# Kernel tuning notes

Measured on AMD Instinct MI355X. Metric: run time of the kernel, lower is better.

Reference implementation:

```python
import jax, jax.numpy as jnp
import numpy as np

D_STATE = 16


def setup_inputs() -> dict:
    key = jax.random.key(0)
    ks = jax.random.split(key, 7)
    B, S, D = 8, 4096, 64
    ds = D_STATE
    x = jax.random.normal(ks[0], (B, S, D), dtype=jnp.float32)
    # Selection layers modeled as Linear(d_model, out). W_A scaled small so the
    # random transition matrices are contractive over 4096 steps.
    W_A = jax.random.normal(ks[1], (D, ds * ds), dtype=jnp.float32) * 0.01
    b_A = jnp.zeros((ds * ds,), dtype=jnp.float32)
    W_B = jax.random.normal(ks[2], (D, ds * D), dtype=jnp.float32) * 0.05
    b_B = jnp.zeros((ds * D,), dtype=jnp.float32)
    W_C = jax.random.normal(ks[3], (D, ds * D), dtype=jnp.float32) * 0.05
    b_C = jnp.zeros((ds * D,), dtype=jnp.float32)
    return {"x": x, "W_A": W_A, "b_A": b_A, "W_B": W_B, "b_B": b_B,
            "W_C": W_C, "b_C": b_C}


def reference(x, W_A, b_A, W_B, b_B, W_C, b_C):
    B, S, D = x.shape
    ds = D_STATE
    # Input-dependent (selective) parameters per timestep
    A = (x @ W_A + b_A).reshape(B, S, ds, ds)      # [B,S,ds,ds]
    Bm = (x @ W_B + b_B).reshape(B, S, ds, D)      # [B,S,ds,D]
    Cm = (x @ W_C + b_C).reshape(B, S, ds, D)      # [B,S,ds,D]
    # Pre-contract B_t @ x_t once: [B,S,ds]
    Bx = jnp.einsum('bsnd,bsd->bsn', Bm, x)

    def step(h, inputs):
        A_t, Bx_t = inputs                          # [B,ds,ds], [B,ds]
        h = jnp.einsum('bij,bj->bi', A_t, h) + Bx_t
        return h, h

    h0 = jnp.zeros((B, ds), dtype=x.dtype)
    _, hs = jax.lax.scan(step, h0,
                         (jnp.swapaxes(A, 0, 1), jnp.swapaxes(Bx, 0, 1)))
    hs = jnp.swapaxes(hs, 0, 1)                     # [B,S,ds]
    # output_t = C_t^T @ h_t  -> [B,S,D]
    return jnp.einsum('bsnd,bsn->bsd', Cm, hs)
```

## Files before the change

### kernel.cpp

```cpp
#include <hip/hip_runtime.h>

#define BATCH   8
#define SEQ     4096
#define DM      64
#define DS      16
#define BS      (BATCH*SEQ)
#define CHUNK   32
#define NCH     (SEQ/CHUNK)
#define NCH_TOT (BATCH*NCH)
#define SG      16
#define NSG     (NCH_TOT/SG)

typedef __attribute__((ext_vector_type(8))) __bf16 bf16x8;
typedef __attribute__((ext_vector_type(4))) float  f32x4;

__device__ __forceinline__ unsigned short f2bf(float f) {
  unsigned int u = __float_as_uint(f);
  u += 0x7fffu + ((u >> 16) & 1u);
  return (unsigned short)(u >> 16);
}
__device__ __forceinline__ float bflo(unsigned int u) { return __uint_as_float(u << 16); }
__device__ __forceinline__ float bfhi(unsigned int u) { return __uint_as_float(u & 0xffff0000u); }

#define AS_I 20
#define AS_T 324

__global__ __launch_bounds__(256) void k0_cast(
    const float* __restrict__ x, const float* __restrict__ WA,
    const float* __restrict__ WB, const float* __restrict__ WC,
    unsigned short* __restrict__ xb, unsigned short* __restrict__ WAt,
    unsigned short* __restrict__ WBt, unsigned short* __restrict__ WCt)
{
  const int b = blockIdx.x;
  if (b < 1024) {
    const int i = (b * 256 + threadIdx.x) * 8;
    float4 v0 = *(const float4*)(x + i);
    float4 v1 = *(const float4*)(x + i + 4);
    ushort4 o0 = {f2bf(v0.x), f2bf(v0.y), f2bf(v0.z), f2bf(v0.w)};
    ushort4 o1 = {f2bf(v1.x), f2bf(v1.y), f2bf(v1.z), f2bf(v1.w)};
    *(ushort4*)(xb + i)     = o0;
    *(ushort4*)(xb + i + 4) = o1;
  } else {
    const int o = (b - 1024) * 256 + threadIdx.x;
    if (o < 16384) {
      const int c = o >> 6, e = o & 63;
      WAt[o] = f2bf(WA[e * 256 + c]);
    } else if (o < 16384 + 65536) {
      const int p = o - 16384;
      const int c = p >> 6, e = p & 63;
      WBt[p] = f2bf(WB[e * 1024 + c]);
    } else {
      const int p = o - 16384 - 65536;
      const int c = p >> 6, e = p & 63;
      WCt[p] = f2bf(WC[e * 1024 + c]);
    }
  }
}

__global__ __launch_bounds__(256) void g1(
    const unsigned short* __restrict__ xb, const unsigned short* __restrict__ WBt,
    const float* __restrict__ bB, const float* __restrict__ x,
    const unsigned short* __restrict__ WAt, const float* __restrict__ bA,
    unsigned short* __restrict__ Wt_ws, float* __restrict__ u_ws,
    float* __restrict__ P_ws, float* __restrict__ v_ws)
{
  __shared__ __align__(16) unsigned char smem[64 * AS_T * 2];
  float (*xs)[68]     = (float (*)[68])smem;
  float* bBs          = (float*)(smem + 17408);
  unsigned short* As  = (unsigned short*)smem;
  __shared__ __align__(16) float bxs[64][16];
  __shared__ __align__(16) float us[2][16];

  const int tid  = threadIdx.x;
  const int lane = tid & 63;
  const int l15  = lane & 15;
  const int quad = lane >> 4;
  const int w    = tid >> 6;
  const int t0   = blockIdx.x * 64;
  const int twl  = w * 16;

  {
    const float4* xg = (const float4*)(x + (size_t)t0 * DM);
    #pragma unroll
    for (int i = 0; i < 4; ++i) {
      const int f4 = tid + 256 * i;
      ((float4*)&xs[f4 >> 4][0])[f4 & 15] = xg[f4];
    }
    ((float4*)bBs)[tid] = ((const float4*)bB)[tid];
    if (tid < 32) us[tid >> 4][tid & 15] = 0.f;
  }

  const bf16x8* xv = (const bf16x8*)(xb + (size_t)(t0 + twl + l15) * 64);
  bf16x8 a0 = xv[quad];
  bf16x8 a1 = xv[quad + 4];
  __syncthreads();

  #pragma unroll 2
  for (int n = 0; n < 16; ++n) {
    f32x4 ac[4];
    #pragma unroll
    for (int r = 0; r < 4; ++r) {
      const bf16x8* wv = (const bf16x8*)(WBt + (size_t)((n * 4 + r) * 16 + l15) * 64);
      f32x4 t = {0.f, 0.f, 0.f, 0.f};
      t = __builtin_amdgcn_mfma_f32_16x16x32_bf16(a0, wv[quad],     t, 0, 0, 0);
      t = __builtin_amdgcn_mfma_f32_16x16x32_bf16(a1, wv[quad + 4], t, 0, 0, 0);
      ac[r] = t;
    }
    float part[4] = {0.f, 0.f, 0.f, 0.f};
    #pragma unroll
    for (int r = 0; r < 4; ++r) {
      const float bb = bBs[n * 64 + r * 16 + l15];
      #pragma unroll
      for (int reg = 0; reg < 4; ++reg) {
        const int tl = twl + quad * 4 + reg;
        part[reg] = fmaf(ac[r][reg] + bb, xs[tl][r * 16 + l15], part[reg]);
      }
    }
    #pragma unroll
    for (int off = 1; off < 16; off <<= 1) {
      #pragma unroll
      for (int reg = 0; reg < 4; ++reg)
        part[reg] += __shfl_xor(part[reg], off, 64);
    }
    if (l15 == 0) {
      #pragma unroll
      for (int reg = 0; reg < 4; ++reg)
        bxs[twl + quad * 4 + reg][n] = part[reg];
    }
  }
  __syncthreads();

  #pragma unroll 2
  for (int ns = 0; ns < 16; ++ns) {
    const bf16x8* wv = (const bf16x8*)(WAt + (size_t)(ns * 16 + l15) * 64);
    f32x4 acc = {0.f, 0.f, 0.f, 0.f};
    acc = __builtin_amdgcn_mfma_f32_16x16x32_bf16(a0, wv[quad],     acc, 0, 0, 0);
    acc = __builtin_amdgcn_mfma_f32_16x16x32_bf16(a1, wv[quad + 4], acc, 0, 0, 0);
    const float bias = bA[ns * 16 + l15];
    #pragma unroll
    for (int r = 0; r < 4; ++r)
      As[(twl + quad * 4 + r) * AS_T + ns * AS_I + l15] = f2bf(acc[r] + bias);
  }
  __syncthreads();

  if (w < 2) {
    const int tb = w * 32;
    bf16x8 wb;
    #pragma unroll
    for (int j = 0; j < 8; ++j) wb[j] = (__bf16)((quad * 8 + j == l15) ? 1.f : 0.f);
    f32x4 d = {0.f, 0.f, 0.f, 0.f};
    const int qq = quad & 1;

    #pragma unroll 1
    for (int t = 0; t < CHUNK; ++t) {
      const int tl = tb + t;
      const unsigned short* rp = &As[tl * AS_T + l15 * AS_I];
      uint2 r0 = *(const uint2*)(rp);
      uint2 r1 = *(const uint2*)(rp + 4);
      uint2 r2 = *(const uint2*)(rp + 8);
      uint2 r3 = *(const uint2*)(rp + 12);

      uint4 abits;
      if (quad == 0)      abits = make_uint4(r0.x, r0.y, r1.x, r1.y);
      else if (quad == 1) abits = make_uint4(r2.x, r2.y, r3.x, r3.y);
      else                abits = make_uint4(0u, 0u, 0u, 0u);
      bf16x8 af = *(bf16x8*)&abits;

      f32x4 z4 = {0.f, 0.f, 0.f, 0.f};
      d = __builtin_amdgcn_mfma_f32_16x16x32_bf16(af, wb, z4, 0, 0, 0);

      float nu = bxs[tl][l15];
      {
        float4 U0 = *(const float4*)&us[w][0];
        float4 U1 = *(const float4*)&us[w][4];
        float4 U2 = *(const float4*)&us[w][8];
        float4 U3 = *(const float4*)&us[w][12];
        nu = fmaf(bflo(r0.x), U0.x, nu); nu = fmaf(bfhi(r0.x), U0.y, nu);
        nu = fmaf(bflo(r0.y), U0.z, nu); nu = fmaf(bfhi(r0.y), U0.w, nu);
        nu = fmaf(bflo(r1.x), U1.x, nu); nu = fmaf(bfhi(r1.x), U1.y, nu);
        nu = fmaf(bflo(r2.x), U2.x, nu); nu = fmaf(bfhi(r2.x), U2.y, nu);
        nu = fmaf(bflo(r2.y), U2.z, nu); nu = fmaf(bfhi(r2.y), U2.w, nu);
        nu = fmaf(bflo(r3.x), U3.x, nu); nu = fmaf(bfhi(r3.x), U3.y, nu);
        nu = fmaf(bflo(r1.y), U1.z, nu); nu = fmaf(bfhi(r1.y), U1.w, nu);
        nu = fmaf(bflo(r3.y), U3.z, nu); nu = fmaf(bfhi(r3.y), U3.w, nu);
      }

      bf16x8 nb;
      nb[0] = (__bf16)__shfl(d[0], (2 * qq + 0) * 16 + l15, 64);
      nb[1] = (__bf16)__shfl(d[1], (2 * qq + 0) * 16 + l15, 64);
      nb[2] = (__bf16)__shfl(d[2], (2 * qq + 0) * 16 + l15, 64);
      nb[3] = (__bf16)__shfl(d[3], (2 * qq + 0) * 16 + l15, 64);
      nb[4] = (__bf16)__shfl(d[0], (2 * qq + 1) * 16 + l15, 64);
      nb[5] = (__bf16)__shfl(d[1], (2 * qq + 1) * 16 + l15, 64);
      nb[6] = (__bf16)__shfl(d[2], (2 * qq + 1) * 16 + l15, 64);
      nb[7] = (__bf16)__shfl(d[3], (2 * qq + 1) * 16 + l15, 64);
      wb = nb;

      if (quad == 0) {
        us[w][l15] = nu;
        u_ws[(size_t)(t0 + tl) * DS + l15] = nu;
      }
      #pragma unroll
      for (int r = 0; r < 4; ++r)
        As[tl * AS_T + (quad * 4 + r) * AS_I + l15] = f2bf(d[r]);
    }

    const int chunk = blockIdx.x * 2 + w;
    #pragma unroll
    for (int r = 0; r < 4; ++r)
      P_ws[(size_t)chunk * 256 + (quad * 4 + r) * 16 + l15] = d[r];
    if (quad == 0) v_ws[(size_t)chunk * DS + l15] = us[w][l15];
  }
  __syncthreads();

  {
    uint4* Wg = (uint4*)(Wt_ws + (size_t)t0 * 256);
    #pragma unroll 1
    for (int z = 0; z < 8; ++z) {
      const int p4 = z * 256 + tid;
      const int f  = p4 * 8;
      const int t  = f >> 8, i = (f >> 4) & 15, k = f & 15;
      const unsigned short* sp = &As[t * AS_T + i * AS_I + k];
      uint2 lo = *(const uint2*)(sp);
      uint2 hi = *(const uint2*)(sp + 4);
      Wg[p4] = make_uint4(lo.x, lo.y, hi.x, hi.y);
    }
  }
}

__global__ __launch_bounds__(256) void k3a(
    const float* __restrict__ P_ws, const float* __restrict__ v_ws,
    float* __restrict__ Q_ws, float* __restrict__ w_ws)
{
  __shared__ float wsv[4][16];
  const int tid  = threadIdx.x;
  const int lane = tid & 63;
  const int l15  = lane & 15;
  const int quad = lane >> 4;
  const int wv   = tid >> 6;
  const int s    = blockIdx.x * 4 + wv;
  const int qq   = quad & 1;

  if (lane < 16) wsv[wv][lane] = 0.f;
  bf16x8 wb;
  #pragma unroll
  for (int j = 0; j < 8; ++j) wb[j] = (__bf16)((quad * 8 + j == l15) ? 1.f : 0.f);
  f32x4 d = {0.f, 0.f, 0.f, 0.f};

  #pragma unroll 1
  for (int t = 0; t < SG; ++t) {
    const int chunk = s * SG + t;
    float4 p0 = {0.f,0.f,0.f,0.f}, p1 = {0.f,0.f,0.f,0.f};
    if (quad < 2) {
      const float4* pr = (const float4*)(P_ws + (size_t)chunk * 256 + l15 * 16 + quad * 8);
      p0 = pr[0]; p1 = pr[1];
    }
    bf16x8 af;
    af[0] = (__bf16)p0.x; af[1] = (__bf16)p0.y; af[2] = (__bf16)p0.z; af[3] = (__bf16)p0.w;
    af[4] = (__bf16)p1.x; af[5] = (__bf16)p1.y; af[6] = (__bf16)p1.z; af[7] = (__bf16)p1.w;

    f32x4 z4 = {0.f, 0.f, 0.f, 0.f};
    d = __builtin_amdgcn_mfma_f32_16x16x32_bf16(af, wb, z4, 0, 0, 0);

    float part = 0.f;
    if (quad < 2) {
      const float* wrow = &wsv[wv][quad * 8];
      part = p0.x*wrow[0] + p0.y*wrow[1] + p0.z*wrow[2] + p0.w*wrow[3]
           + p1.x*wrow[4] + p1.y*wrow[5] + p1.z*wrow[6] + p1.w*wrow[7];
    }
    part += __shfl_xor(part, 16, 64);
    const float nv = v_ws[(size_t)chunk * DS + l15];

    bf16x8 nb;
    nb[0] = (__bf16)__shfl(d[0], (2 * qq + 0) * 16 + l15, 64);
    nb[1] = (__bf16)__shfl(d[1], (2 * qq + 0) * 16 + l15, 64);
    nb[2] = (__bf16)__shfl(d[2], (2 * qq + 0) * 16 + l15, 64);
    nb[3] = (__bf16)__shfl(d[3], (2 * qq + 0) * 16 + l15, 64);
    nb[4] = (__bf16)__shfl(d[0], (2 * qq + 1) * 16 + l15, 64);
    nb[5] = (__bf16)__shfl(d[1], (2 * qq + 1) * 16 + l15, 64);
    nb[6] = (__bf16)__shfl(d[2], (2 * qq + 1) * 16 + l15, 64);
    nb[7] = (__bf16)__shfl(d[3], (2 * qq + 1) * 16 + l15, 64);
    wb = nb;

    if (quad == 0) wsv[wv][l15] = part + nv;
  }

  #pragma unroll
  for (int r = 0; r < 4; ++r)
    Q_ws[(size_t)s * 256 + (quad * 4 + r) * 16 + l15] = d[r];
  if (quad == 0) w_ws[(size_t)s * DS + l15] = wsv[wv][l15];
}

__global__ __launch_bounds__(128) void k3b(
    const float* __restrict__ Q_ws, const float* __restrict__ w_ws,
    float* __restrict__ hbg_ws)
{
  const int tid = threadIdx.x;
  const int b = tid >> 4;
  const int r = tid & 15;
  float h = 0.f;

  #pragma unroll 1
  for (int g = 0; g < 8; ++g) {
    const int s = b * 8 + g;
    const float4* Pr = (const float4*)&Q_ws[(size_t)s * 256 + r * 16];
    float4 c0 = Pr[0], c1 = Pr[1], c2 = Pr[2], c3 = Pr[3];
    const float vc = w_ws[(size_t)s * DS + r];
    hbg_ws[(size_t)s * DS + r] = h;
    float acc = vc;
    acc += c0.x*__shfl(h, 0,16) + c0.y*__shfl(h, 1,16) + c0.z*__shfl(h, 2,16) + c0.w*__shfl(h, 3,16);
    acc += c1.x*__shfl(h, 4,16) + c1.y*__shfl(h, 5,16) + c1.z*__shfl(h, 6,16) + c1.w*__shfl(h, 7,16);
    acc += c2.x*__shfl(h, 8,16) + c2.y*__shfl(h, 9,16) + c2.z*__shfl(h,10,16) + c2.w*__shfl(h,11,16);
    acc += c3.x*__shfl(h,12,16) + c3.y*__shfl(h,13,16) + c3.z*__shfl(h,14,16) + c3.w*__shfl(h,15,16);
    h = acc;
  }
}

__global__ __launch_bounds__(256) void k3c(
    const float* __restrict__ P_ws, const float* __restrict__ v_ws,
    const float* __restrict__ hbg_ws, float* __restrict__ hb_ws)
{
  const int tid = threadIdx.x;
  const int s = blockIdx.x * 16 + (tid >> 4);
  const int r = tid & 15;
  float h = hbg_ws[(size_t)s * DS + r];

  #pragma unroll 1
  for (int t = 0; t < SG; ++t) {
    const int chunk = s * SG + t;
    const float4* Pr = (const float4*)&P_ws[(size_t)chunk * 256 + r * 16];
    float4 c0 = Pr[0], c1 = Pr[1], c2 = Pr[2], c3 = Pr[3];
    const float vc = v_ws[(size_t)chunk * DS + r];
    hb_ws[(size_t)chunk * DS + r] = h;
    float acc = vc;
    acc += c0.x*__shfl(h, 0,16) + c0.y*__shfl(h, 1,16) + c0.z*__shfl(h, 2,16) + c0.w*__shfl(h, 3,16);
    acc += c1.x*__shfl(h, 4,16) + c1.y*__shfl(h, 5,16) + c1.z*__shfl(h, 6,16) + c1.w*__shfl(h, 7,16);
    acc += c2.x*__shfl(h, 8,16) + c2.y*__shfl(h, 9,16) + c2.z*__shfl(h,10,16) + c2.w*__shfl(h,11,16);
    acc += c3.x*__shfl(h,12,16) + c3.y*__shfl(h,13,16) + c3.z*__shfl(h,14,16) + c3.w*__shfl(h,15,16);
    h = acc;
  }
}

__global__ __launch_bounds__(256) void g2(
    const unsigned short* __restrict__ xb, const unsigned short* __restrict__ WCt,
    const float* __restrict__ bC, const unsigned short* __restrict__ Wt_ws,
    const float* __restrict__ u_ws, const float* __restrict__ hb_ws,
    float* __restrict__ out)
{
  __shared__ float hsh[64][17];
  __shared__ float bCs[1024];
  const int tid  = threadIdx.x;
  const int lane = tid & 63;
  const int l15  = lane & 15;
  const int quad = lane >> 4;
  const int w    = tid >> 6;
  const int t0   = blockIdx.x * 64;
  const int twl  = w * 16;

  ((float4*)bCs)[tid] = ((const float4*)bC)[tid];

  #pragma unroll
  for (int z = 0; z < 4; ++z) {
    const int gcell = z * 256 + tid;
    const int tl = gcell >> 4, i = gcell & 15;
    const int t = t0 + tl;
    const uint4* wr = (const uint4*)(Wt_ws + (size_t)t * 256 + i * 16);
    uint4 wa = wr[0], wbv = wr[1];
    const float4* hp = (const float4*)(hb_ws + (size_t)(t >> 5) * DS);
    float4 h0 = hp[0], h1 = hp[1], h2 = hp[2], h3 = hp[3];
    float acc = u_ws[(size_t)t * DS + i];
    acc = fmaf(bflo(wa.x),  h0.x, acc); acc = fmaf(bfhi(wa.x),  h0.y, acc);
    acc = fmaf(bflo(wa.y),  h0.z, acc); acc = fmaf(bfhi(wa.y),  h0.w, acc);
    acc = fmaf(bflo(wa.z),  h1.x, acc); acc = fmaf(bfhi(wa.z),  h1.y, acc);
    acc = fmaf(bflo(wa.w),  h1.z, acc); acc = fmaf(bfhi(wa.w),  h1.w, acc);
    acc = fmaf(bflo(wbv.x), h2.x, acc); acc = fmaf(bfhi(wbv.x), h2.y, acc);
    acc = fmaf(bflo(wbv.y), h2.z, acc); acc = fmaf(bfhi(wbv.y), h2.w, acc);
    acc = fmaf(bflo(wbv.z), h3.x, acc); acc = fmaf(bfhi(wbv.z), h3.y, acc);
    acc = fmaf(bflo(wbv.w), h3.z, acc); acc = fmaf(bfhi(wbv.w), h3.w, acc);
    hsh[tl][i] = acc;
  }

  const bf16x8* xv = (const bf16x8*)(xb + (size_t)(t0 + twl + l15) * 64);
  bf16x8 a0 = xv[quad];
  bf16x8 a1 = xv[quad + 4];
  __syncthreads();

  f32x4 ota[4];
  #pragma unroll
  for (int r = 0; r < 4; ++r) ota[r] = (f32x4){0.f, 0.f, 0.f, 0.f};

  #pragma unroll 2
  for (int n = 0; n < 16; ++n) {
    f32x4 ac[4];
    #pragma unroll
    for (int r = 0; r < 4; ++r) {
      const bf16x8* wv = (const bf16x8*)(WCt + (size_t)((n * 4 + r) * 16 + l15) * 64);
      f32x4 t = {0.f, 0.f, 0.f, 0.f};
      t = __builtin_amdgcn_mfma_f32_16x16x32_bf16(a0, wv[quad],     t, 0, 0, 0);
      t = __builtin_amdgcn_mfma_f32_16x16x32_bf16(a1, wv[quad + 4], t, 0, 0, 0);
      ac[r] = t;
    }
    float hn[4];
    #pragma unroll
    for (int reg = 0; reg < 4; ++reg) hn[reg] = hsh[twl + quad * 4 + reg][n];
    #pragma unroll
    for (int r = 0; r < 4; ++r) {
      const float bc = bCs[n * 64 + r * 16 + l15];
      #pragma unroll
      for (int reg = 0; reg < 4; ++reg)
        ota[r][reg] = fmaf(ac[r][reg] + bc, hn[reg], ota[r][reg]);
    }
  }

  #pragma unroll
  for (int r = 0; r < 4; ++r)
    #pragma unroll
    for (int reg = 0; reg < 4; ++reg)
      out[(size_t)(t0 + twl + quad * 4 + reg) * DM + r * 16 + l15] = ota[r][reg];
}

extern "C" void kernel_launch(void* const* d_in, const int* in_sizes, int n_in,
                              void* d_out, int out_size, void* d_ws, size_t ws_size,
                              hipStream_t stream) {
  const float* x  = (const float*)d_in[0];
  const float* WA = (const float*)d_in[1];
  const float* bA = (const float*)d_in[2];
  const float* WB = (const float*)d_in[3];
  const float* bB = (const float*)d_in[4];
  const float* WC = (const float*)d_in[5];
  const float* bC = (const float*)d_in[6];
  float* out = (float*)d_out;

  float* ws     = (float*)d_ws;
  float* P_ws   = ws;
  float* v_ws   = P_ws   + (size_t)NCH_TOT * 256;
  float* u_ws   = v_ws   + (size_t)NCH_TOT * DS;
  float* Q_ws   = u_ws   + (size_t)BS * DS;
  float* w_ws   = Q_ws   + (size_t)NSG * 256;
  float* hbg_ws = w_ws   + (size_t)NSG * DS;
  float* hb_ws  = hbg_ws + (size_t)NSG * DS;
  unsigned short* xb    = (unsigned short*)(hb_ws + (size_t)NCH_TOT * DS);
  unsigned short* WAt   = xb  + (size_t)BS * 64;
  unsigned short* WBt   = WAt + 256 * 64;
  unsigned short* WCt   = WBt + 1024 * 64;
  unsigned short* Wt_ws = WCt + 1024 * 64;

  k0_cast <<<1600,    256, 0, stream>>>(x, WA, WB, WC, xb, WAt, WBt, WCt);
  g1      <<<BS / 64, 256, 0, stream>>>(xb, WBt, bB, x, WAt, bA, Wt_ws, u_ws, P_ws, v_ws);
  k3a     <<<NSG / 4, 256, 0, stream>>>(P_ws, v_ws, Q_ws, w_ws);
  k3b     <<<1,       128, 0, stream>>>(Q_ws, w_ws, hbg_ws);
  k3c     <<<4,       256, 0, stream>>>(P_ws, v_ws, hbg_ws, hb_ws);
  g2      <<<BS / 64, 256, 0, stream>>>(xb, WCt, bC, Wt_ws, u_ws, hb_ws, out);
}
```

Measured before the change: 185.6 us.

## Halve scan chunk size and fuse x bf16 cast into g1

After: 181.8 us. 2.0% less time.

```diff
diff --git a/kernel.cpp b/kernel.cpp
--- a/kernel.cpp
+++ b/kernel.cpp
@@ -5,11 +5,10 @@
 #define DM      64
 #define DS      16
 #define BS      (BATCH*SEQ)
-#define CHUNK   32
-#define NCH     (SEQ/CHUNK)
-#define NCH_TOT (BATCH*NCH)
+#define CHUNK   16
+#define NCHT    (BS/CHUNK)
 #define SG      16
-#define NSG     (NCH_TOT/SG)
+#define NSG     (NCHT/SG)
 
 typedef __attribute__((ext_vector_type(8))) __bf16 bf16x8;
 typedef __attribute__((ext_vector_type(4))) float  f32x4;
@@ -25,50 +24,39 @@
 #define AS_I 20
 #define AS_T 324
 
-__global__ __launch_bounds__(256) void k0_cast(
-    const float* __restrict__ x, const float* __restrict__ WA,
-    const float* __restrict__ WB, const float* __restrict__ WC,
-    unsigned short* __restrict__ xb, unsigned short* __restrict__ WAt,
-    unsigned short* __restrict__ WBt, unsigned short* __restrict__ WCt)
-{
-  const int b = blockIdx.x;
-  if (b < 1024) {
-    const int i = (b * 256 + threadIdx.x) * 8;
-    float4 v0 = *(const float4*)(x + i);
-    float4 v1 = *(const float4*)(x + i + 4);
-    ushort4 o0 = {f2bf(v0.x), f2bf(v0.y), f2bf(v0.z), f2bf(v0.w)};
-    ushort4 o1 = {f2bf(v1.x), f2bf(v1.y), f2bf(v1.z), f2bf(v1.w)};
-    *(ushort4*)(xb + i)     = o0;
-    *(ushort4*)(xb + i + 4) = o1;
+__global__ __launch_bounds__(256) void k0_castw(
+    const float* __restrict__ WA, const float* __restrict__ WB,
+    const float* __restrict__ WC,
+    unsigned short* __restrict__ WAt, unsigned short* __restrict__ WBt,
+    unsigned short* __restrict__ WCt)
+{
+  const int o = blockIdx.x * 256 + threadIdx.x;
+  if (o < 16384) {
+    const int c = o >> 6, e = o & 63;
+    WAt[o] = f2bf(WA[e * 256 + c]);
+  } else if (o < 16384 + 65536) {
+    const int p = o - 16384;
+    const int c = p >> 6, e = p & 63;
+    WBt[p] = f2bf(WB[e * 1024 + c]);
   } else {
-    const int o = (b - 1024) * 256 + threadIdx.x;
-    if (o < 16384) {
-      const int c = o >> 6, e = o & 63;
-      WAt[o] = f2bf(WA[e * 256 + c]);
-    } else if (o < 16384 + 65536) {
-      const int p = o - 16384;
-      const int c = p >> 6, e = p & 63;
-      WBt[p] = f2bf(WB[e * 1024 + c]);
-    } else {
-      const int p = o - 16384 - 65536;
-      const int c = p >> 6, e = p & 63;
-      WCt[p] = f2bf(WC[e * 1024 + c]);
-    }
-  }
-}
-
-__global__ __launch_bounds__(256) void g1(
-    const unsigned short* __restrict__ xb, const unsigned short* __restrict__ WBt,
-    const float* __restrict__ bB, const float* __restrict__ x,
-    const unsigned short* __restrict__ WAt, const float* __restrict__ bA,
+    const int p = o - 16384 - 65536;
+    const int c = p >> 6, e = p & 63;
+    WCt[p] = f2bf(WC[e * 1024 + c]);
+  }
+}
+
+__global__ __launch_bounds__(128) void g1(
+    const float* __restrict__ x, const unsigned short* __restrict__ WBt,
+    const float* __restrict__ bB, const unsigned short* __restrict__ WAt,
+    const float* __restrict__ bA, unsigned short* __restrict__ xb,
     unsigned short* __restrict__ Wt_ws, float* __restrict__ u_ws,
     float* __restrict__ P_ws, float* __restrict__ v_ws)
 {
-  __shared__ __align__(16) unsigned char smem[64 * AS_T * 2];
+  __shared__ __align__(16) unsigned char smem[32 * AS_T * 2];
   float (*xs)[68]     = (float (*)[68])smem;
-  float* bBs          = (float*)(smem + 17408);
+  float* bBs          = (float*)(smem + 8704);
   unsigned short* As  = (unsigned short*)smem;
-  __shared__ __align__(16) float bxs[64][16];
+  __shared__ __align__(16) float bxs[32][16];
   __shared__ __align__(16) float us[2][16];
 
   const int tid  = threadIdx.x;
@@ -76,24 +64,39 @@
   const int l15  = lane & 15;
   const int quad = lane >> 4;
   const int w    = tid >> 6;
-  const int t0   = blockIdx.x * 64;
+  const int t0   = blockIdx.x * 32;
   const int twl  = w * 16;
 
   {
     const float4* xg = (const float4*)(x + (size_t)t0 * DM);
     #pragma unroll
     for (int i = 0; i < 4; ++i) {
-      const int f4 = tid + 256 * i;
+      const int f4 = tid + 128 * i;
       ((float4*)&xs[f4 >> 4][0])[f4 & 15] = xg[f4];
     }
-    ((float4*)bBs)[tid] = ((const float4*)bB)[tid];
+    ((float4*)bBs)[tid]       = ((const float4*)bB)[tid];
+    ((float4*)bBs)[tid + 128] = ((const float4*)bB)[tid + 128];
     if (tid < 32) us[tid >> 4][tid & 15] = 0.f;
   }
-
-  const bf16x8* xv = (const bf16x8*)(xb + (size_t)(t0 + twl + l15) * 64);
-  bf16x8 a0 = xv[quad];
-  bf16x8 a1 = xv[quad + 4];
   __syncthreads();
+
+  bf16x8 a0, a1;
+  {
+    const int row = twl + l15;
+    union { bf16x8 v; ushort4 s[2]; } ua, ub;
+    float4 p0 = *(const float4*)&xs[row][quad * 8];
+    float4 p1 = *(const float4*)&xs[row][quad * 8 + 4];
+    float4 p2 = *(const float4*)&xs[row][32 + quad * 8];
+    float4 p3 = *(const float4*)&xs[row][32 + quad * 8 + 4];
+    ua.s[0] = (ushort4){f2bf(p0.x), f2bf(p0.y), f2bf(p0.z), f2bf(p0.w)};
+    ua.s[1] = (ushort4){f2bf(p1.x), f2bf(p1.y), f2bf(p1.z), f2bf(p1.w)};
+    ub.s[0] = (ushort4){f2bf(p2.x), f2bf(p2.y), f2bf(p2.z), f2bf(p2.w)};
+    ub.s[1] = (ushort4){f2bf(p3.x), f2bf(p3.y), f2bf(p3.z), f2bf(p3.w)};
+    a0 = ua.v; a1 = ub.v;
+    unsigned short* xp = xb + (size_t)(t0 + row) * 64 + quad * 8;
+    *(bf16x8*)xp        = a0;
+    *(bf16x8*)(xp + 32) = a1;
+  }
 
   #pragma unroll 2
   for (int n = 0; n < 16; ++n) {
@@ -143,8 +146,7 @@
   }
   __syncthreads();
 
-  if (w < 2) {
-    const int tb = w * 32;
+  {
     bf16x8 wb;
     #pragma unroll
     for (int j = 0; j < 8; ++j) wb[j] = (__bf16)((quad * 8 + j == l15) ? 1.f : 0.f);
@@ -153,7 +155,7 @@
 
     #pragma unroll 1
     for (int t = 0; t < CHUNK; ++t) {
-      const int tl = tb + t;
+      const int tl = twl + t;
       const unsigned short* rp = &As[tl * AS_T + l15 * AS_I];
       uint2 r0 = *(const uint2*)(rp);
       uint2 r1 = *(const uint2*)(rp + 4);
@@ -178,10 +180,10 @@
         nu = fmaf(bflo(r0.x), U0.x, nu); nu = fmaf(bfhi(r0.x), U0.y, nu);
         nu = fmaf(bflo(r0.y), U0.z, nu); nu = fmaf(bfhi(r0.y), U0.w, nu);
         nu = fmaf(bflo(r1.x), U1.x, nu); nu = fmaf(bfhi(r1.x), U1.y, nu);
+        nu = fmaf(bflo(r1.y), U1.z, nu); nu = fmaf(bfhi(r1.y), U1.w, nu);
         nu = fmaf(bflo(r2.x), U2.x, nu); nu = fmaf(bfhi(r2.x), U2.y, nu);
         nu = fmaf(bflo(r2.y), U2.z, nu); nu = fmaf(bfhi(r2.y), U2.w, nu);
         nu = fmaf(bflo(r3.x), U3.x, nu); nu = fmaf(bfhi(r3.x), U3.y, nu);
-        nu = fmaf(bflo(r1.y), U1.z, nu); nu = fmaf(bfhi(r1.y), U1.w, nu);
         nu = fmaf(bflo(r3.y), U3.z, nu); nu = fmaf(bfhi(r3.y), U3.w, nu);
       }
 
@@ -198,7 +200,7 @@
 
       if (quad == 0) {
         us[w][l15] = nu;
-        u_ws[(size_t)(t0 + tl) * DS + l15] = nu;
+        bxs[tl][l15] = nu;
       }
       #pragma unroll
       for (int r = 0; r < 4; ++r)
@@ -217,7 +219,7 @@
     uint4* Wg = (uint4*)(Wt_ws + (size_t)t0 * 256);
     #pragma unroll 1
     for (int z = 0; z < 8; ++z) {
-      const int p4 = z * 256 + tid;
+      const int p4 = z * 128 + tid;
       const int f  = p4 * 8;
       const int t  = f >> 8, i = (f >> 4) & 15, k = f & 15;
       const unsigned short* sp = &As[t * AS_T + i * AS_I + k];
@@ -225,6 +227,7 @@
       uint2 hi = *(const uint2*)(sp + 4);
       Wg[p4] = make_uint4(lo.x, lo.y, hi.x, hi.y);
     }
+    ((float4*)(u_ws + (size_t)t0 * DS))[tid] = ((const float4*)&bxs[0][0])[tid];
   }
 }
 
@@ -301,8 +304,8 @@
   float h = 0.f;
 
   #pragma unroll 1
-  for (int g = 0; g < 8; ++g) {
-    const int s = b * 8 + g;
+  for (int g = 0; g < 16; ++g) {
+    const int s = b * 16 + g;
     const float4* Pr = (const float4*)&Q_ws[(size_t)s * 256 + r * 16];
     float4 c0 = Pr[0], c1 = Pr[1], c2 = Pr[2], c3 = Pr[3];
     const float vc = w_ws[(size_t)s * DS + r];
@@ -366,7 +369,7 @@
     const int t = t0 + tl;
     const uint4* wr = (const uint4*)(Wt_ws + (size_t)t * 256 + i * 16);
     uint4 wa = wr[0], wbv = wr[1];
-    const float4* hp = (const float4*)(hb_ws + (size_t)(t >> 5) * DS);
+    const float4* hp = (const float4*)(hb_ws + (size_t)(t >> 4) * DS);
     float4 h0 = hp[0], h1 = hp[1], h2 = hp[2], h3 = hp[3];
     float acc = u_ws[(size_t)t * DS + i];
     acc = fmaf(bflo(wa.x),  h0.x, acc); acc = fmaf(bfhi(wa.x),  h0.y, acc);
@@ -433,22 +436,22 @@
 
   float* ws     = (float*)d_ws;
   float* P_ws   = ws;
-  float* v_ws   = P_ws   + (size_t)NCH_TOT * 256;
-  float* u_ws   = v_ws   + (size_t)NCH_TOT * DS;
+  float* v_ws   = P_ws   + (size_t)NCHT * 256;
+  float* u_ws   = v_ws   + (size_t)NCHT * DS;
   float* Q_ws   = u_ws   + (size_t)BS * DS;
   float* w_ws   = Q_ws   + (size_t)NSG * 256;
   float* hbg_ws = w_ws   + (size_t)NSG * DS;
   float* hb_ws  = hbg_ws + (size_t)NSG * DS;
-  unsigned short* xb    = (unsigned short*)(hb_ws + (size_t)NCH_TOT * DS);
+  unsigned short* xb    = (unsigned short*)(hb_ws + (size_t)NCHT * DS);
   unsigned short* WAt   = xb  + (size_t)BS * 64;
   unsigned short* WBt   = WAt + 256 * 64;
   unsigned short* WCt   = WBt + 1024 * 64;
   unsigned short* Wt_ws = WCt + 1024 * 64;
 
-  k0_cast <<<1600,    256, 0, stream>>>(x, WA, WB, WC, xb, WAt, WBt, WCt);
-  g1      <<<BS / 64, 256, 0, stream>>>(xb, WBt, bB, x, WAt, bA, Wt_ws, u_ws, P_ws, v_ws);
-  k3a     <<<NSG / 4, 256, 0, stream>>>(P_ws, v_ws, Q_ws, w_ws);
-  k3b     <<<1,       128, 0, stream>>>(Q_ws, w_ws, hbg_ws);
-  k3c     <<<4,       256, 0, stream>>>(P_ws, v_ws, hbg_ws, hb_ws);
-  g2      <<<BS / 64, 256, 0, stream>>>(xb, WCt, bC, Wt_ws, u_ws, hb_ws, out);
-}
+  k0_castw<<<576,      256, 0, stream>>>(WA, WB, WC, WAt, WBt, WCt);
+  g1      <<<BS / 32,  128, 0, stream>>>(x, WBt, bB, WAt, bA, xb, Wt_ws, u_ws, P_ws, v_ws);
+  k3a     <<<NSG / 4,  256, 0, stream>>>(P_ws, v_ws, Q_ws, w_ws);
+  k3b     <<<1,        128, 0, stream>>>(Q_ws, w_ws, hbg_ws);
+  k3c     <<<NSG / 16, 256, 0, stream>>>(P_ws, v_ws, hbg_ws, hb_ws);
+  g2      <<<BS / 64,  256, 0, stream>>>(xb, WCt, bC, Wt_ws, u_ws, hb_ws, out);
+}
```
